# Performance work log

Measured on AMD Instinct MI355X. Metric: run time of the kernel, lower is better.

Reference implementation:

```python
import jax, jax.numpy as jnp
import numpy as np

# NF4 (NormalFloat4) codebook from bitsandbytes
NF4 = jnp.array([
    -1.0, -0.6961928009986877, -0.5250730514526367, -0.39491748809814453,
    -0.28444138169288635, -0.18477343022823334, -0.09105003625154495, 0.0,
    0.07958029955625534, 0.16093020141124725, 0.24611230194568634,
    0.33791524171829224, 0.44070982933044434, 0.5626170039176941,
    0.7229568362236023, 1.0], dtype=jnp.float32)

BLOCK = 64          # bnb default quantization block size
RANK = 8
ALPHA = 16
SCALING = ALPHA / RANK


def setup_inputs() -> dict:
    key = jax.random.key(0)
    k = jax.random.split(key, 6)
    B, S, I, O = 4, 2048, 4096, 4096
    x = jax.random.normal(k[0], (B, S, I), dtype=jnp.float32)
    w_codes = jax.random.randint(k[1], (O, I), 0, 16, dtype=jnp.int32)
    absmax = jax.random.uniform(k[2], (O, I // BLOCK), dtype=jnp.float32)
    bias = jax.random.normal(k[3], (O,), dtype=jnp.float32)
    lora_A = jax.random.normal(k[4], (I, RANK), dtype=jnp.float32) / np.sqrt(I)
    lora_B = jax.random.normal(k[5], (RANK, O), dtype=jnp.float32)
    return {"x": x, "w_codes": w_codes, "absmax": absmax, "bias": bias,
            "lora_A": lora_A, "lora_B": lora_B}


def reference(x, w_codes, absmax, bias, lora_A, lora_B):
    O, I = w_codes.shape
    # NF4 dequantize: code lookup scaled by per-block absmax -> W [O, I]
    W = (NF4[w_codes].reshape(O, I // BLOCK, BLOCK) * absmax[:, :, None]).reshape(O, I)
    base = jnp.einsum('bsi,oi->bso', x, W) + bias
    # low-rank LoRA branch (dropout=0 -> identity)
    lora = ((x @ lora_A) @ lora_B) * SCALING
    return base + lora
```

## Files before the change

kernel.cpp:

```cpp
#include <hip/hip_runtime.h>
#include <hip/hip_bf16.h>
#include <stdint.h>


typedef __bf16 bf16x8 __attribute__((ext_vector_type(8)));
typedef float  f32x4  __attribute__((ext_vector_type(4)));
typedef unsigned short u16x8 __attribute__((ext_vector_type(8)));

__constant__ float NF4_TAB[16] = {
    -1.0f, -0.6961928009986877f, -0.5250730514526367f, -0.39491748809814453f,
    -0.28444138169288635f, -0.18477343022823334f, -0.09105003625154495f, 0.0f,
    0.07958029955625534f, 0.16093020141124725f, 0.24611230194568634f,
    0.33791524171829224f, 0.44070982933044434f, 0.5626170039176941f,
    0.7229568362236023f, 1.0f};

__device__ __forceinline__ unsigned short f2bf(float f) {
    unsigned int u = __float_as_uint(f);
    u += 0x7FFFu + ((u >> 16) & 1u);
    return (unsigned short)(u >> 16);
}

__global__ __launch_bounds__(256) void prep_kernel(
    const float* __restrict__ x, unsigned short* __restrict__ xb, int n8, int nCvt,
    const int* __restrict__ codes, const float* __restrict__ absmax,
    const float* __restrict__ lA, const float* __restrict__ lB,
    unsigned short* __restrict__ W, int O, int I, int nIb) {
    if ((int)blockIdx.x < nCvt) {
        int i = blockIdx.x * 256 + threadIdx.x;
        if (i >= n8) return;
        const float4* p = (const float4*)x + (long)i * 2;
        float4 a = p[0], b = p[1];
        u16x8 o;
        o[0] = f2bf(a.x); o[1] = f2bf(a.y); o[2] = f2bf(a.z); o[3] = f2bf(a.w);
        o[4] = f2bf(b.x); o[5] = f2bf(b.y); o[6] = f2bf(b.z); o[7] = f2bf(b.w);
        *((u16x8*)xb + i) = o;
    } else {
        const int b2 = blockIdx.x - nCvt;
        const int o  = b2 / nIb;
        const int i0 = (b2 - o * nIb) * 2048 + threadIdx.x * 8;
        float bo[8];
#pragma unroll
        for (int r = 0; r < 8; ++r) bo[r] = lB[(long)r * O + o] * 2.0f;
        const long base = (long)o * I + i0;
        const int4* cp = (const int4*)(codes + base);
        int4 c0 = cp[0], c1 = cp[1];
        const float am = absmax[o * (I >> 6) + (i0 >> 6)];
        int cc[8] = {c0.x, c0.y, c0.z, c0.w, c1.x, c1.y, c1.z, c1.w};
        u16x8 ov;
#pragma unroll
        for (int j = 0; j < 8; ++j) {
            const float4* ap = (const float4*)(lA + (long)(i0 + j) * 8);
            float4 a0 = ap[0], a1 = ap[1];
            float w = NF4_TAB[cc[j] & 15] * am;
            w += a0.x * bo[0] + a0.y * bo[1] + a0.z * bo[2] + a0.w * bo[3]
               + a1.x * bo[4] + a1.y * bo[5] + a1.z * bo[6] + a1.w * bo[7];
            ov[j] = f2bf(w);
        }
        *(u16x8*)(W + base) = ov;
    }
}

#define BM 256
#define BN 256
#define BK 64

#define GLOAD16(g, s) __builtin_amdgcn_global_load_lds(                     \
    (const __attribute__((address_space(1))) void*)(g),                     \
    (__attribute__((address_space(3))) void*)(s), 16, 0, 0)

#define STAGE(ptr, ldsbase) do {                                            \
    GLOAD16((ptr), (char*)(ldsbase) + ldsW);                                \
    GLOAD16((ptr) + SK, (char*)(ldsbase) + 8192 + ldsW); } while (0)

#define BAR() do { asm volatile("" ::: "memory");                           \
    __builtin_amdgcn_s_barrier(); asm volatile("" ::: "memory"); } while (0)

#define MFMA_QUAD(H, KQ, BREG)                                              \
    _Pragma("unroll") for (int mi = 0; mi < 4; ++mi)                        \
    _Pragma("unroll") for (int ni = 0; ni < 2; ++ni) {                      \
        acc[H][KQ][mi][ni] = __builtin_amdgcn_mfma_f32_16x16x32_bf16(       \
            a[mi][0], BREG[ni][0], acc[H][KQ][mi][ni], 0, 0, 0);            \
        acc[H][KQ][mi][ni] = __builtin_amdgcn_mfma_f32_16x16x32_bf16(       \
            a[mi][1], BREG[ni][1], acc[H][KQ][mi][ni], 0, 0, 0); }

__global__ __launch_bounds__(512, 2) void gemm_kernel(
    const unsigned short* __restrict__ A,
    const unsigned short* __restrict__ Bm,
    const float* __restrict__ bias,
    float* __restrict__ out, int M, int N, int K, int gx, int gy) {
    __shared__ char lds[2][65536];

    int bx, by;
    {
        const int bid = blockIdx.x;
        if ((gx & 7) == 0 && (gy & 7) == 0 && ((gx >> 3) * (gy >> 3)) == 8) {
            const int xcd = bid & 7, loc = bid >> 3;
            const int cxs = gx >> 3;
            const int cr = xcd / cxs, cc = xcd - cr * cxs;
            by = cr * 8 + (loc >> 3);
            bx = cc * 8 + (loc & 7);
        } else if (((gx * gy) & 7) == 0) {
            const int q = (gx * gy) >> 3;
            const int id = (bid & 7) * q + (bid >> 3);
            bx = id % gx; by = id / gx;
        } else { bx = bid % gx; by = bid / gx; }
    }

    const int t = threadIdx.x;
    const int w = t >> 6, l = t & 63;
    const int wr = w >> 2, wc = w & 3;
    const long mB = (long)by * BM;
    const long nB = (long)bx * BN;
    const int NT = K / BK;

    const int sRow = w * 8 + (l >> 3);
    const int sCol = ((l & 7) ^ (l >> 3)) << 3;
    const int ldsW = w * 1024;
    const long SK = 64L * K;
    const long HK = 128L * K;
    const unsigned short* gA = A  + (mB + sRow) * K + sCol;
    const unsigned short* gB = Bm + (nB + sRow) * K + sCol;

    const unsigned short* pA1 = gA + HK + BK;
    const unsigned short* pB1 = gB + HK + BK;
    const unsigned short* pA0 = gA + 2 * BK;
    const unsigned short* pB0 = gB + 2 * BK;

    const int fr = l & 15;
    const int aoff0 = fr * 128 + ((((l >> 4)) ^ (l & 7)) << 4);
    const int aoff1 = fr * 128 + (((4 + (l >> 4)) ^ (l & 7)) << 4);

    f32x4 acc[2][2][4][2];
#pragma unroll
    for (int h = 0; h < 2; ++h)
#pragma unroll
        for (int k = 0; k < 2; ++k)
#pragma unroll
            for (int mi = 0; mi < 4; ++mi)
#pragma unroll
                for (int ni = 0; ni < 2; ++ni)
                    acc[h][k][mi][ni] = (f32x4){0.f, 0.f, 0.f, 0.f};

    STAGE(gA,      lds[0] + 0);
    STAGE(gA + HK, lds[0] + 16384);
    STAGE(gB,      lds[0] + 32768);
    STAGE(gB + HK, lds[0] + 49152);
    STAGE(gA + BK, lds[1] + 0);
    STAGE(gB + BK, lds[1] + 32768);
    asm volatile("s_waitcnt vmcnt(4)" ::: "memory");
    BAR();

    bf16x8 a[4][2], b0[2][2], b1[2][2];

    for (int g = 0; g < NT; ++g) {
        char* cur = lds[g & 1];
        char* nxt = lds[(g & 1) ^ 1];
        const char* Ab = cur + wr * 8192;
        const char* Bb = cur + 32768 + wc * 4096;
        const bool st1 = (g + 1 < NT), st2 = (g + 2 < NT);

#pragma unroll
        for (int mi = 0; mi < 4; ++mi) {
            a[mi][0] = *(const bf16x8*)(Ab + mi * 2048 + aoff0);
            a[mi][1] = *(const bf16x8*)(Ab + mi * 2048 + aoff1);
        }
#pragma unroll
        for (int ni = 0; ni < 2; ++ni) {
            b0[ni][0] = *(const bf16x8*)(Bb + ni * 2048 + aoff0);
            b0[ni][1] = *(const bf16x8*)(Bb + ni * 2048 + aoff1);
        }
        if (st1) STAGE(pA1, nxt + 16384);
        asm volatile("s_waitcnt vmcnt(6)" ::: "memory");
        BAR();
        __builtin_amdgcn_s_setprio(1);
        MFMA_QUAD(0, 0, b0);
        __builtin_amdgcn_s_setprio(0);

#pragma unroll
        for (int ni = 0; ni < 2; ++ni) {
            b1[ni][0] = *(const bf16x8*)(Bb + 16384 + ni * 2048 + aoff0);
            b1[ni][1] = *(const bf16x8*)(Bb + 16384 + ni * 2048 + aoff1);
        }
        if (st1) STAGE(pB1, nxt + 49152);
        BAR();
        __builtin_amdgcn_s_setprio(1);
        MFMA_QUAD(0, 1, b1);
        __builtin_amdgcn_s_setprio(0);

#pragma unroll
        for (int mi = 0; mi < 4; ++mi) {
            a[mi][0] = *(const bf16x8*)(Ab + 16384 + mi * 2048 + aoff0);
            a[mi][1] = *(const bf16x8*)(Ab + 16384 + mi * 2048 + aoff1);
        }
        if (st2) STAGE(pA0, cur + 0);
        BAR();
        __builtin_amdgcn_s_setprio(1);
        MFMA_QUAD(1, 0, b0);
        __builtin_amdgcn_s_setprio(0);

        if (st2) STAGE(pB0, cur + 32768);
        if (st2) { asm volatile("s_waitcnt vmcnt(8)" ::: "memory"); }
        else     { asm volatile("s_waitcnt vmcnt(0)" ::: "memory"); }
        BAR();
        __builtin_amdgcn_s_setprio(1);
        MFMA_QUAD(1, 1, b1);
        __builtin_amdgcn_s_setprio(0);

        pA1 += BK; pB1 += BK; pA0 += BK; pB0 += BK;
    }

    const int r4 = (l >> 4) * 4;
#pragma unroll
    for (int kq = 0; kq < 2; ++kq) {
        float bs[2];
#pragma unroll
        for (int ni = 0; ni < 2; ++ni)
            bs[ni] = bias[nB + kq * 128 + wc * 32 + ni * 16 + fr];
#pragma unroll
        for (int h = 0; h < 2; ++h)
#pragma unroll
            for (int mi = 0; mi < 4; ++mi)
#pragma unroll
                for (int r = 0; r < 4; ++r) {
                    long row = mB + h * 128 + wr * 64 + mi * 16 + r4 + r;
                    float* op = out + row * N + nB + kq * 128 + wc * 32 + fr;
#pragma unroll
                    for (int ni = 0; ni < 2; ++ni)
                        op[ni * 16] = acc[h][kq][mi][ni][r] + bs[ni];
                }
    }
}

__global__ void naive_kernel(const float* __restrict__ x, const int* __restrict__ codes,
                             const float* __restrict__ absmax, const float* __restrict__ bias,
                             const float* __restrict__ lA, const float* __restrict__ lB,
                             float* __restrict__ out, int M, int I, int O) {
    long idx = (long)blockIdx.x * 256 + threadIdx.x;
    if (idx >= (long)M * O) return;
    int o = (int)(idx % O);
    long m = idx / O;
    const float* xr = x + m * I;
    const int* cr = codes + (long)o * I;
    const float* ar = absmax + (long)o * (I >> 6);
    float acc = 0.f;
    float la[8] = {0, 0, 0, 0, 0, 0, 0, 0};
    for (int i = 0; i < I; ++i) {
        float xv = xr[i];
        acc += xv * NF4_TAB[cr[i] & 15] * ar[i >> 6];
        const float* av = lA + (long)i * 8;
#pragma unroll
        for (int r = 0; r < 8; ++r) la[r] += xv * av[r];
    }
    float lv = 0.f;
#pragma unroll
    for (int r = 0; r < 8; ++r) lv += la[r] * lB[(long)r * O + o];
    out[idx] = acc + bias[o] + 2.0f * lv;
}

extern "C" void kernel_launch(void* const* d_in, const int* in_sizes, int n_in,
                              void* d_out, int out_size, void* d_ws, size_t ws_size,
                              hipStream_t stream) {
    const float* x      = (const float*)d_in[0];
    const int*   codes  = (const int*)d_in[1];
    const float* absmax = (const float*)d_in[2];
    const float* bias   = (const float*)d_in[3];
    const float* lA     = (const float*)d_in[4];
    const float* lB     = (const float*)d_in[5];
    float* out = (float*)d_out;

    const int I = in_sizes[4] / 8;
    const int O = in_sizes[3];
    const int M = in_sizes[0] / I;
    const int K = I;

    const size_t need = (size_t)M * K * 2 + (size_t)O * K * 2;
    if (ws_size < need || (M % BM) || (O % BN) || (K % 2048) || (K / BK) < 2) {
        long tot = (long)M * O;
        naive_kernel<<<(int)((tot + 255) / 256), 256, 0, stream>>>(
            x, codes, absmax, bias, lA, lB, out, M, I, O);
        return;
    }

    unsigned short* xb = (unsigned short*)d_ws;
    unsigned short* wb = xb + (size_t)M * K;

    const int n8   = (M * K) / 8;
    const int nCvt = (n8 + 255) / 256;
    const int nIb  = K / 2048;
    const int nPrep = nCvt + O * nIb;
    prep_kernel<<<nPrep, 256, 0, stream>>>(x, xb, n8, nCvt,
                                           codes, absmax, lA, lB, wb, O, K, nIb);
    const int gx = O / BN, gy = M / BM;
    gemm_kernel<<<gx * gy, 512, 0, stream>>>(xb, wb, bias, out, M, O, K, gx, gy);
}
```

Measured before the change: 353.2 us.

## Switch GEMM to 32x32x16 MFMA tiles and grid-stride the prep kernel

Each wave's GEMM subtile is now computed with 32x32x16 bf16 MFMA instructions instead of 16x16x32. This halves the instruction count per tile and changes the LDS fragment addressing and the epilogue's output row mapping. The prep kernel also moves from one block per chunk to a fixed grid of grid-stride blocks, and each convert thread now handles 16 floats. The aim is higher MFMA throughput and fewer prep launch blocks. The risks are LDS bank conflicts under the new swizzle offsets and less parallelism in the prep kernel.

```diff
diff --git a/kernel.cpp b/kernel.cpp
--- a/kernel.cpp
+++ b/kernel.cpp
@@ -4,7 +4,7 @@
 
 
 typedef __bf16 bf16x8 __attribute__((ext_vector_type(8)));
-typedef float  f32x4  __attribute__((ext_vector_type(4)));
+typedef float  f32x16 __attribute__((ext_vector_type(16)));
 typedef unsigned short u16x8 __attribute__((ext_vector_type(8)));
 
 __constant__ float NF4_TAB[16] = {
@@ -20,43 +20,51 @@
     return (unsigned short)(u >> 16);
 }
 
+#define CVT_BLOCKS 2048
+#define BLD_BLOCKS 2048
+
 __global__ __launch_bounds__(256) void prep_kernel(
-    const float* __restrict__ x, unsigned short* __restrict__ xb, int n8, int nCvt,
+    const float* __restrict__ x, unsigned short* __restrict__ xb, int n16,
     const int* __restrict__ codes, const float* __restrict__ absmax,
     const float* __restrict__ lA, const float* __restrict__ lB,
-    unsigned short* __restrict__ W, int O, int I, int nIb) {
-    if ((int)blockIdx.x < nCvt) {
-        int i = blockIdx.x * 256 + threadIdx.x;
-        if (i >= n8) return;
-        const float4* p = (const float4*)x + (long)i * 2;
-        float4 a = p[0], b = p[1];
-        u16x8 o;
-        o[0] = f2bf(a.x); o[1] = f2bf(a.y); o[2] = f2bf(a.z); o[3] = f2bf(a.w);
-        o[4] = f2bf(b.x); o[5] = f2bf(b.y); o[6] = f2bf(b.z); o[7] = f2bf(b.w);
-        *((u16x8*)xb + i) = o;
+    unsigned short* __restrict__ W, int O, int I, int nIb, int nChunks) {
+    if ((int)blockIdx.x < CVT_BLOCKS) {
+        for (int i = blockIdx.x * 256 + threadIdx.x; i < n16;
+             i += CVT_BLOCKS * 256) {
+            const float4* p = (const float4*)x + (long)i * 4;
+            float4 a = p[0], b = p[1], c = p[2], d = p[3];
+            u16x8 o0, o1;
+            o0[0] = f2bf(a.x); o0[1] = f2bf(a.y); o0[2] = f2bf(a.z); o0[3] = f2bf(a.w);
+            o0[4] = f2bf(b.x); o0[5] = f2bf(b.y); o0[6] = f2bf(b.z); o0[7] = f2bf(b.w);
+            o1[0] = f2bf(c.x); o1[1] = f2bf(c.y); o1[2] = f2bf(c.z); o1[3] = f2bf(c.w);
+            o1[4] = f2bf(d.x); o1[5] = f2bf(d.y); o1[6] = f2bf(d.z); o1[7] = f2bf(d.w);
+            ((u16x8*)xb)[(long)i * 2]     = o0;
+            ((u16x8*)xb)[(long)i * 2 + 1] = o1;
+        }
     } else {
-        const int b2 = blockIdx.x - nCvt;
-        const int o  = b2 / nIb;
-        const int i0 = (b2 - o * nIb) * 2048 + threadIdx.x * 8;
-        float bo[8];
-#pragma unroll
-        for (int r = 0; r < 8; ++r) bo[r] = lB[(long)r * O + o] * 2.0f;
-        const long base = (long)o * I + i0;
-        const int4* cp = (const int4*)(codes + base);
-        int4 c0 = cp[0], c1 = cp[1];
-        const float am = absmax[o * (I >> 6) + (i0 >> 6)];
-        int cc[8] = {c0.x, c0.y, c0.z, c0.w, c1.x, c1.y, c1.z, c1.w};
-        u16x8 ov;
-#pragma unroll
-        for (int j = 0; j < 8; ++j) {
-            const float4* ap = (const float4*)(lA + (long)(i0 + j) * 8);
-            float4 a0 = ap[0], a1 = ap[1];
-            float w = NF4_TAB[cc[j] & 15] * am;
-            w += a0.x * bo[0] + a0.y * bo[1] + a0.z * bo[2] + a0.w * bo[3]
-               + a1.x * bo[4] + a1.y * bo[5] + a1.z * bo[6] + a1.w * bo[7];
-            ov[j] = f2bf(w);
+        for (int b2 = blockIdx.x - CVT_BLOCKS; b2 < nChunks; b2 += BLD_BLOCKS) {
+            const int o  = b2 / nIb;
+            const int i0 = (b2 - o * nIb) * 2048 + threadIdx.x * 8;
+            float bo[8];
+#pragma unroll
+            for (int r = 0; r < 8; ++r) bo[r] = lB[(long)r * O + o] * 2.0f;
+            const long base = (long)o * I + i0;
+            const int4* cp = (const int4*)(codes + base);
+            int4 c0 = cp[0], c1 = cp[1];
+            const float am = absmax[o * (I >> 6) + (i0 >> 6)];
+            int cc[8] = {c0.x, c0.y, c0.z, c0.w, c1.x, c1.y, c1.z, c1.w};
+            u16x8 ov;
+#pragma unroll
+            for (int j = 0; j < 8; ++j) {
+                const float4* ap = (const float4*)(lA + (long)(i0 + j) * 8);
+                float4 a0 = ap[0], a1 = ap[1];
+                float w = NF4_TAB[cc[j] & 15] * am;
+                w += a0.x * bo[0] + a0.y * bo[1] + a0.z * bo[2] + a0.w * bo[3]
+                   + a1.x * bo[4] + a1.y * bo[5] + a1.z * bo[6] + a1.w * bo[7];
+                ov[j] = f2bf(w);
+            }
+            *(u16x8*)(W + base) = ov;
         }
-        *(u16x8*)(W + base) = ov;
     }
 }
 
@@ -75,13 +83,11 @@
 #define BAR() do { asm volatile("" ::: "memory");                           \
     __builtin_amdgcn_s_barrier(); asm volatile("" ::: "memory"); } while (0)
 
-#define MFMA_QUAD(H, KQ, BREG)                                              \
-    _Pragma("unroll") for (int mi = 0; mi < 4; ++mi)                        \
-    _Pragma("unroll") for (int ni = 0; ni < 2; ++ni) {                      \
-        acc[H][KQ][mi][ni] = __builtin_amdgcn_mfma_f32_16x16x32_bf16(       \
-            a[mi][0], BREG[ni][0], acc[H][KQ][mi][ni], 0, 0, 0);            \
-        acc[H][KQ][mi][ni] = __builtin_amdgcn_mfma_f32_16x16x32_bf16(       \
-            a[mi][1], BREG[ni][1], acc[H][KQ][mi][ni], 0, 0, 0); }
+#define MFMA_OCT(H, KQ, BREG)                                               \
+    _Pragma("unroll") for (int kk = 0; kk < 4; ++kk)                        \
+    _Pragma("unroll") for (int mb = 0; mb < 2; ++mb)                        \
+        acc[H][KQ][mb] = __builtin_amdgcn_mfma_f32_32x32x16_bf16(           \
+            a[mb][kk], BREG[kk], acc[H][KQ][mb], 0, 0, 0);
 
 __global__ __launch_bounds__(512, 2) void gemm_kernel(
     const unsigned short* __restrict__ A,
@@ -126,20 +132,24 @@
     const unsigned short* pA0 = gA + 2 * BK;
     const unsigned short* pB0 = gB + 2 * BK;
 
-    const int fr = l & 15;
-    const int aoff0 = fr * 128 + ((((l >> 4)) ^ (l & 7)) << 4);
-    const int aoff1 = fr * 128 + (((4 + (l >> 4)) ^ (l & 7)) << 4);
-
-    f32x4 acc[2][2][4][2];
+    const int fr = l & 31;
+    const int kb = l >> 5;
+    int c4[4];
+#pragma unroll
+    for (int kk = 0; kk < 4; ++kk)
+        c4[kk] = ((kb + 2 * kk) ^ (fr & 7)) << 4;
+    const int aRow = (wr * 64 + fr) * 128;
+    const int bRow = (wc * 32 + fr) * 128;
+
+    f32x16 acc[2][2][2];
 #pragma unroll
     for (int h = 0; h < 2; ++h)
 #pragma unroll
-        for (int k = 0; k < 2; ++k)
-#pragma unroll
-            for (int mi = 0; mi < 4; ++mi)
-#pragma unroll
-                for (int ni = 0; ni < 2; ++ni)
-                    acc[h][k][mi][ni] = (f32x4){0.f, 0.f, 0.f, 0.f};
+        for (int kq = 0; kq < 2; ++kq)
+#pragma unroll
+            for (int mb = 0; mb < 2; ++mb)
+#pragma unroll
+                for (int r = 0; r < 16; ++r) acc[h][kq][mb][r] = 0.f;
 
     STAGE(gA,      lds[0] + 0);
     STAGE(gA + HK, lds[0] + 16384);
@@ -150,52 +160,45 @@
     asm volatile("s_waitcnt vmcnt(4)" ::: "memory");
     BAR();
 
-    bf16x8 a[4][2], b0[2][2], b1[2][2];
+    bf16x8 a[2][4], b0[4], b1[4];
 
     for (int g = 0; g < NT; ++g) {
         char* cur = lds[g & 1];
         char* nxt = lds[(g & 1) ^ 1];
-        const char* Ab = cur + wr * 8192;
-        const char* Bb = cur + 32768 + wc * 4096;
         const bool st1 = (g + 1 < NT), st2 = (g + 2 < NT);
 
 #pragma unroll
-        for (int mi = 0; mi < 4; ++mi) {
-            a[mi][0] = *(const bf16x8*)(Ab + mi * 2048 + aoff0);
-            a[mi][1] = *(const bf16x8*)(Ab + mi * 2048 + aoff1);
-        }
-#pragma unroll
-        for (int ni = 0; ni < 2; ++ni) {
-            b0[ni][0] = *(const bf16x8*)(Bb + ni * 2048 + aoff0);
-            b0[ni][1] = *(const bf16x8*)(Bb + ni * 2048 + aoff1);
+        for (int kk = 0; kk < 4; ++kk) {
+#pragma unroll
+            for (int mb = 0; mb < 2; ++mb)
+                a[mb][kk] = *(const bf16x8*)(cur + aRow + mb * 4096 + c4[kk]);
+            b0[kk] = *(const bf16x8*)(cur + 32768 + bRow + c4[kk]);
         }
         if (st1) STAGE(pA1, nxt + 16384);
         asm volatile("s_waitcnt vmcnt(6)" ::: "memory");
         BAR();
         __builtin_amdgcn_s_setprio(1);
-        MFMA_QUAD(0, 0, b0);
-        __builtin_amdgcn_s_setprio(0);
-
-#pragma unroll
-        for (int ni = 0; ni < 2; ++ni) {
-            b1[ni][0] = *(const bf16x8*)(Bb + 16384 + ni * 2048 + aoff0);
-            b1[ni][1] = *(const bf16x8*)(Bb + 16384 + ni * 2048 + aoff1);
-        }
+        MFMA_OCT(0, 0, b0);
+        __builtin_amdgcn_s_setprio(0);
+
+#pragma unroll
+        for (int kk = 0; kk < 4; ++kk)
+            b1[kk] = *(const bf16x8*)(cur + 32768 + 16384 + bRow + c4[kk]);
         if (st1) STAGE(pB1, nxt + 49152);
         BAR();
         __builtin_amdgcn_s_setprio(1);
-        MFMA_QUAD(0, 1, b1);
-        __builtin_amdgcn_s_setprio(0);
-
-#pragma unroll
-        for (int mi = 0; mi < 4; ++mi) {
-            a[mi][0] = *(const bf16x8*)(Ab + 16384 + mi * 2048 + aoff0);
-            a[mi][1] = *(const bf16x8*)(Ab + 16384 + mi * 2048 + aoff1);
-        }
+        MFMA_OCT(0, 1, b1);
+        __builtin_amdgcn_s_setprio(0);
+
+#pragma unroll
+        for (int kk = 0; kk < 4; ++kk)
+#pragma unroll
+            for (int mb = 0; mb < 2; ++mb)
+                a[mb][kk] = *(const bf16x8*)(cur + 16384 + aRow + mb * 4096 + c4[kk]);
         if (st2) STAGE(pA0, cur + 0);
         BAR();
         __builtin_amdgcn_s_setprio(1);
-        MFMA_QUAD(1, 0, b0);
+        MFMA_OCT(1, 0, b0);
         __builtin_amdgcn_s_setprio(0);
 
         if (st2) STAGE(pB0, cur + 32768);
@@ -203,31 +206,27 @@
         else     { asm volatile("s_waitcnt vmcnt(0)" ::: "memory"); }
         BAR();
         __builtin_amdgcn_s_setprio(1);
-        MFMA_QUAD(1, 1, b1);
+        MFMA_OCT(1, 1, b1);
         __builtin_amdgcn_s_setprio(0);
 
         pA1 += BK; pB1 += BK; pA0 += BK; pB0 += BK;
     }
 
-    const int r4 = (l >> 4) * 4;
 #pragma unroll
     for (int kq = 0; kq < 2; ++kq) {
-        float bs[2];
-#pragma unroll
-        for (int ni = 0; ni < 2; ++ni)
-            bs[ni] = bias[nB + kq * 128 + wc * 32 + ni * 16 + fr];
+        const float bs = bias[nB + kq * 128 + wc * 32 + fr];
 #pragma unroll
         for (int h = 0; h < 2; ++h)
 #pragma unroll
-            for (int mi = 0; mi < 4; ++mi)
-#pragma unroll
-                for (int r = 0; r < 4; ++r) {
-                    long row = mB + h * 128 + wr * 64 + mi * 16 + r4 + r;
-                    float* op = out + row * N + nB + kq * 128 + wc * 32 + fr;
-#pragma unroll
-                    for (int ni = 0; ni < 2; ++ni)
-                        op[ni * 16] = acc[h][kq][mi][ni][r] + bs[ni];
+            for (int mb = 0; mb < 2; ++mb) {
+#pragma unroll
+                for (int r = 0; r < 16; ++r) {
+                    long row = mB + h * 128 + wr * 64 + mb * 32
+                             + (r & 3) + 8 * (r >> 2) + 4 * kb;
+                    out[row * N + nB + kq * 128 + wc * 32 + fr] =
+                        acc[h][kq][mb][r] + bs;
                 }
+            }
     }
 }
 
@@ -284,12 +283,11 @@
     unsigned short* xb = (unsigned short*)d_ws;
     unsigned short* wb = xb + (size_t)M * K;
 
-    const int n8   = (M * K) / 8;
-    const int nCvt = (n8 + 255) / 256;
-    const int nIb  = K / 2048;
-    const int nPrep = nCvt + O * nIb;
-    prep_kernel<<<nPrep, 256, 0, stream>>>(x, xb, n8, nCvt,
-                                           codes, absmax, lA, lB, wb, O, K, nIb);
+    const int n16 = (M * K) / 16;
+    const int nIb = K / 2048;
+    const int nChunks = O * nIb;
+    prep_kernel<<<CVT_BLOCKS + BLD_BLOCKS, 256, 0, stream>>>(
+        x, xb, n16, codes, absmax, lA, lB, wb, O, K, nIb, nChunks);
     const int gx = O / BN, gy = M / BM;
     gemm_kernel<<<gx * gy, 512, 0, stream>>>(xb, wb, bias, out, M, O, K, gx, gy);
 }
```

New measurement: 382.1 us. 8.2% more time.

## Fuse fp32-to-bf16 activation conversion into GEMM A-tile loading

Applied to the files above, without the earlier changes.

The separate pass that converted x to bf16 in workspace is removed. The GEMM now loads fp32 activations into registers, converts them, and writes bf16 to LDS, while the weight tiles still use direct global-to-LDS loads. This saves a full read and write of the large activation tensor and one prep kernel, and the weight-build kernel becomes a grid-stride launch. In exchange the GEMM reads twice as many bytes for A on every tile reload, needs extra VGPRs for the in-flight float4 values, and relies on implicit waits in place of the explicit vmcnt pipeline waits.

```diff
diff --git a/kernel.cpp b/kernel.cpp
--- a/kernel.cpp
+++ b/kernel.cpp
@@ -20,22 +20,18 @@
     return (unsigned short)(u >> 16);
 }
 
-__global__ __launch_bounds__(256) void prep_kernel(
-    const float* __restrict__ x, unsigned short* __restrict__ xb, int n8, int nCvt,
+__device__ __forceinline__ u16x8 cvt8(float4 a, float4 b) {
+    u16x8 o;
+    o[0] = f2bf(a.x); o[1] = f2bf(a.y); o[2] = f2bf(a.z); o[3] = f2bf(a.w);
+    o[4] = f2bf(b.x); o[5] = f2bf(b.y); o[6] = f2bf(b.z); o[7] = f2bf(b.w);
+    return o;
+}
+
+__global__ __launch_bounds__(256) void build_w_kernel(
     const int* __restrict__ codes, const float* __restrict__ absmax,
     const float* __restrict__ lA, const float* __restrict__ lB,
-    unsigned short* __restrict__ W, int O, int I, int nIb) {
-    if ((int)blockIdx.x < nCvt) {
-        int i = blockIdx.x * 256 + threadIdx.x;
-        if (i >= n8) return;
-        const float4* p = (const float4*)x + (long)i * 2;
-        float4 a = p[0], b = p[1];
-        u16x8 o;
-        o[0] = f2bf(a.x); o[1] = f2bf(a.y); o[2] = f2bf(a.z); o[3] = f2bf(a.w);
-        o[4] = f2bf(b.x); o[5] = f2bf(b.y); o[6] = f2bf(b.z); o[7] = f2bf(b.w);
-        *((u16x8*)xb + i) = o;
-    } else {
-        const int b2 = blockIdx.x - nCvt;
+    unsigned short* __restrict__ W, int O, int I, int nIb, int nChunks) {
+    for (int b2 = blockIdx.x; b2 < nChunks; b2 += gridDim.x) {
         const int o  = b2 / nIb;
         const int i0 = (b2 - o * nIb) * 2048 + threadIdx.x * 8;
         float bo[8];
@@ -72,6 +68,15 @@
     GLOAD16((ptr), (char*)(ldsbase) + ldsW);                                \
     GLOAD16((ptr) + SK, (char*)(ldsbase) + 8192 + ldsW); } while (0)
 
+#define A_ISSUE(v, p) do {                                                  \
+    (v)[0] = *(const float4*)(p);                                           \
+    (v)[1] = *(const float4*)((p) + 4);                                     \
+    (v)[2] = *(const float4*)((p) + SKf);                                   \
+    (v)[3] = *(const float4*)((p) + SKf + 4); } while (0)
+#define A_WRITE(v, base) do {                                               \
+    *(u16x8*)((char*)(base) + ldsW + l * 16)        = cvt8((v)[0], (v)[1]); \
+    *(u16x8*)((char*)(base) + 8192 + ldsW + l * 16) = cvt8((v)[2], (v)[3]); } while (0)
+
 #define BAR() do { asm volatile("" ::: "memory");                           \
     __builtin_amdgcn_s_barrier(); asm volatile("" ::: "memory"); } while (0)
 
@@ -84,7 +89,7 @@
             a[mi][1], BREG[ni][1], acc[H][KQ][mi][ni], 0, 0, 0); }
 
 __global__ __launch_bounds__(512, 2) void gemm_kernel(
-    const unsigned short* __restrict__ A,
+    const float* __restrict__ X,
     const unsigned short* __restrict__ Bm,
     const float* __restrict__ bias,
     float* __restrict__ out, int M, int N, int K, int gx, int gy) {
@@ -116,15 +121,16 @@
     const int sRow = w * 8 + (l >> 3);
     const int sCol = ((l & 7) ^ (l >> 3)) << 3;
     const int ldsW = w * 1024;
-    const long SK = 64L * K;
-    const long HK = 128L * K;
-    const unsigned short* gA = A  + (mB + sRow) * K + sCol;
-    const unsigned short* gB = Bm + (nB + sRow) * K + sCol;
-
-    const unsigned short* pA1 = gA + HK + BK;
-    const unsigned short* pB1 = gB + HK + BK;
-    const unsigned short* pA0 = gA + 2 * BK;
-    const unsigned short* pB0 = gB + 2 * BK;
+    const long SK  = 64L * K;
+    const long SKf = 64L * K;
+    const long HK  = 128L * K;
+    const float*          gAf = X  + (mB + sRow) * K + sCol;
+    const unsigned short* gB  = Bm + (nB + sRow) * K + sCol;
+
+    const float*          pA1f = gAf + HK + BK;
+    const float*          pA0f = gAf + 2 * BK;
+    const unsigned short* pB1  = gB + HK + BK;
+    const unsigned short* pB0  = gB + 2 * BK;
 
     const int fr = l & 15;
     const int aoff0 = fr * 128 + ((((l >> 4)) ^ (l & 7)) << 4);
@@ -141,13 +147,19 @@
                 for (int ni = 0; ni < 2; ++ni)
                     acc[h][k][mi][ni] = (f32x4){0.f, 0.f, 0.f, 0.f};
 
-    STAGE(gA,      lds[0] + 0);
-    STAGE(gA + HK, lds[0] + 16384);
     STAGE(gB,      lds[0] + 32768);
     STAGE(gB + HK, lds[0] + 49152);
-    STAGE(gA + BK, lds[1] + 0);
     STAGE(gB + BK, lds[1] + 32768);
-    asm volatile("s_waitcnt vmcnt(4)" ::: "memory");
+    {
+        float4 v0[4], v1[4], v2[4];
+        A_ISSUE(v0, gAf);
+        A_ISSUE(v1, gAf + HK);
+        A_ISSUE(v2, gAf + BK);
+        A_WRITE(v0, lds[0] + 0);
+        A_WRITE(v1, lds[0] + 16384);
+        A_WRITE(v2, lds[1] + 0);
+    }
+    asm volatile("s_waitcnt vmcnt(0) lgkmcnt(0)" ::: "memory");
     BAR();
 
     bf16x8 a[4][2], b0[2][2], b1[2][2];
@@ -158,6 +170,7 @@
         const char* Ab = cur + wr * 8192;
         const char* Bb = cur + 32768 + wc * 4096;
         const bool st1 = (g + 1 < NT), st2 = (g + 2 < NT);
+        float4 va1[4], va0[4];
 
 #pragma unroll
         for (int mi = 0; mi < 4; ++mi) {
@@ -169,8 +182,7 @@
             b0[ni][0] = *(const bf16x8*)(Bb + ni * 2048 + aoff0);
             b0[ni][1] = *(const bf16x8*)(Bb + ni * 2048 + aoff1);
         }
-        if (st1) STAGE(pA1, nxt + 16384);
-        asm volatile("s_waitcnt vmcnt(6)" ::: "memory");
+        if (st1) A_ISSUE(va1, pA1f);
         BAR();
         __builtin_amdgcn_s_setprio(1);
         MFMA_QUAD(0, 0, b0);
@@ -181,7 +193,10 @@
             b1[ni][0] = *(const bf16x8*)(Bb + 16384 + ni * 2048 + aoff0);
             b1[ni][1] = *(const bf16x8*)(Bb + 16384 + ni * 2048 + aoff1);
         }
-        if (st1) STAGE(pB1, nxt + 49152);
+        if (st1) {
+            STAGE(pB1, nxt + 49152);
+            A_WRITE(va1, nxt + 16384);
+        }
         BAR();
         __builtin_amdgcn_s_setprio(1);
         MFMA_QUAD(0, 1, b1);
@@ -192,21 +207,24 @@
             a[mi][0] = *(const bf16x8*)(Ab + 16384 + mi * 2048 + aoff0);
             a[mi][1] = *(const bf16x8*)(Ab + 16384 + mi * 2048 + aoff1);
         }
-        if (st2) STAGE(pA0, cur + 0);
+        if (st2) A_ISSUE(va0, pA0f);
         BAR();
         __builtin_amdgcn_s_setprio(1);
         MFMA_QUAD(1, 0, b0);
         __builtin_amdgcn_s_setprio(0);
 
-        if (st2) STAGE(pB0, cur + 32768);
-        if (st2) { asm volatile("s_waitcnt vmcnt(8)" ::: "memory"); }
-        else     { asm volatile("s_waitcnt vmcnt(0)" ::: "memory"); }
+        if (st2) {
+            STAGE(pB0, cur + 32768);
+            A_WRITE(va0, cur + 0);
+        } else {
+            asm volatile("s_waitcnt vmcnt(0)" ::: "memory");
+        }
         BAR();
         __builtin_amdgcn_s_setprio(1);
         MFMA_QUAD(1, 1, b1);
         __builtin_amdgcn_s_setprio(0);
 
-        pA1 += BK; pB1 += BK; pA0 += BK; pB0 += BK;
+        pA1f += BK; pA0f += BK; pB1 += BK; pB0 += BK;
     }
 
     const int r4 = (l >> 4) * 4;
@@ -273,7 +291,7 @@
     const int M = in_sizes[0] / I;
     const int K = I;
 
-    const size_t need = (size_t)M * K * 2 + (size_t)O * K * 2;
+    const size_t need = (size_t)O * K * 2;
     if (ws_size < need || (M % BM) || (O % BN) || (K % 2048) || (K / BK) < 2) {
         long tot = (long)M * O;
         naive_kernel<<<(int)((tot + 255) / 256), 256, 0, stream>>>(
@@ -281,15 +299,12 @@
         return;
     }
 
-    unsigned short* xb = (unsigned short*)d_ws;
-    unsigned short* wb = xb + (size_t)M * K;
-
-    const int n8   = (M * K) / 8;
-    const int nCvt = (n8 + 255) / 256;
-    const int nIb  = K / 2048;
-    const int nPrep = nCvt + O * nIb;
-    prep_kernel<<<nPrep, 256, 0, stream>>>(x, xb, n8, nCvt,
-                                           codes, absmax, lA, lB, wb, O, K, nIb);
+    unsigned short* wb = (unsigned short*)d_ws;
+
+    const int nIb = K / 2048;
+    const int nChunks = O * nIb;
+    build_w_kernel<<<2048, 256, 0, stream>>>(codes, absmax, lA, lB, wb,
+                                             O, K, nIb, nChunks);
     const int gx = O / BN, gy = M / BM;
-    gemm_kernel<<<gx * gy, 512, 0, stream>>>(xb, wb, bias, out, M, O, K, gx, gy);
-}
+    gemm_kernel<<<gx * gy, 512, 0, stream>>>(x, wb, bias, out, M, O, K, gx, gy);
+}
```

Result: slower. 645.2 us (+82.7%).
